# Kernel optimization log

Hardware: AMD Instinct MI355X
Metric: run time of the kernel (lower is better)

Reference implementation:

```python
import jax, jax.numpy as jnp
import numpy as np

N = 65536   # total sentences
B = 8192    # number of bags (ragged scopes)
C = 1024    # class_dim
R = 100     # rel_num


def setup_inputs() -> dict:
    key = jax.random.key(0)
    k1, k2, k3, k4 = jax.random.split(key, 4)
    X = jax.random.normal(k1, (N, C), jnp.float32)            # post-fc1 sentence reps
    Constraints = jax.random.normal(k2, (R, C), jnp.float32)  # post-fc2 constraint reps
    W = jax.random.normal(k3, (R, C), jnp.float32) * 0.02     # classifier weight
    b = jnp.zeros((R,), jnp.float32)                           # classifier bias
    # ragged scopes: random cut points -> contiguous [start, end) per bag
    rng = np.random.default_rng(0)
    cuts = np.sort(rng.choice(np.arange(1, N), B - 1, replace=False))
    starts = np.concatenate([[0], cuts])
    ends = np.concatenate([cuts, [N]])
    X_Scope = jnp.asarray(np.stack([starts, ends], axis=1), jnp.int32)  # [B, 2]
    X_Rel = jax.random.randint(k4, (B,), 0, R, jnp.int32)               # [B]
    return dict(X=X, Constraints=Constraints, W=W, b=b, X_Scope=X_Scope, X_Rel=X_Rel)


def reference(X, Constraints, W, b, X_Scope, X_Rel):
    n, _ = X.shape
    nb = X_Scope.shape[0]
    # map each sentence to its (contiguous) bag via scope starts
    starts = X_Scope[:, 0]
    seg = jnp.searchsorted(starts, jnp.arange(n, dtype=starts.dtype), side='right') - 1  # [N]
    # per-sentence attention logit against its bag's relation constraint
    Con = Constraints[X_Rel]                                   # [B, C]
    scores = jnp.einsum('nc,nc->n', X, Con[seg])               # [N]
    # numerically-stable per-bag softmax
    m = jax.ops.segment_max(scores, seg, num_segments=nb)      # [B]
    e = jnp.exp(scores - m[seg])                               # [N]
    denom = jax.ops.segment_sum(e, seg, num_segments=nb)       # [B]
    w = e / denom[seg]                                         # [N]
    # attention-weighted bag pooling
    bag = jax.ops.segment_sum(w[:, None] * X, seg, num_segments=nb)  # [B, C]
    # classifier (dropout is identity at eval)
    return bag @ W.T + b                                       # [B, R]
```

## Files before the change

### kernel.cpp

```cpp
#include <hip/hip_runtime.h>
#include <math.h>

#define CDIM 1024
#define RDIM 100
#define NBAGS 8192

typedef float floatx4 __attribute__((ext_vector_type(4)));
typedef short bf16x8 __attribute__((ext_vector_type(8)));

__device__ __forceinline__ float dot4(float4 a, float4 b) {
    return a.x * b.x + a.y * b.y + a.z * b.z + a.w * b.w;
}

__device__ __forceinline__ unsigned short f2bf(float f) {
    unsigned int u = __builtin_bit_cast(unsigned int, f);
    u += 0x7FFFu + ((u >> 16) & 1u);
    return (unsigned short)(u >> 16);
}

__global__ __launch_bounds__(256) void bag_softmax_kernel(
    const float* __restrict__ X,
    const float* __restrict__ Constraints,
    const int* __restrict__ scope,
    const int* __restrict__ rel,
    const float* __restrict__ W,
    unsigned short* __restrict__ bagbuf,
    unsigned short* __restrict__ Wbf)
{
    const int lane = threadIdx.x & 63;
    const int w    = threadIdx.x >> 6;

    if (blockIdx.x >= NBAGS) {
        const int rr = blockIdx.x - NBAGS;
        const int t  = threadIdx.x;
        float4 v = *(const float4*)(W + (size_t)rr * CDIM + t * 4);
        ushort4 o;
        o.x = f2bf(v.x); o.y = f2bf(v.y); o.z = f2bf(v.z); o.w = f2bf(v.w);
        *(ushort4*)(Wbf + (size_t)rr * CDIM + t * 4) = o;
        return;
    }

    __shared__ float4 lds_acc[4][256];
    __shared__ float  lds_m[4];
    __shared__ float  lds_d[4];

    const int bag = blockIdx.x;
    const int s = scope[2 * bag];
    const int e = scope[2 * bag + 1];
    const int r = rel[bag];

    const float4* conp = (const float4*)(Constraints + (size_t)r * CDIM);
    const float4 c0 = conp[lane];
    const float4 c1 = conp[lane + 64];
    const float4 c2 = conp[lane + 128];
    const float4 c3 = conp[lane + 192];

    float4 a0 = {0.f, 0.f, 0.f, 0.f};
    float4 a1 = {0.f, 0.f, 0.f, 0.f};
    float4 a2 = {0.f, 0.f, 0.f, 0.f};
    float4 a3 = {0.f, 0.f, 0.f, 0.f};
    float m = -INFINITY;
    float denom = 0.f;

    int row = s + w;
    if (row < e) {
        const float4* xp = (const float4*)(X + (size_t)row * CDIM);
        float4 A0 = xp[lane];
        float4 A1 = xp[lane + 64];
        float4 A2 = xp[lane + 128];
        float4 A3 = xp[lane + 192];

        for (; row < e; row += 4) {
            const int nxt = (row + 4 < e) ? (row + 4) : row;
            const float4* np = (const float4*)(X + (size_t)nxt * CDIM);
            float4 B0 = np[lane];
            float4 B1 = np[lane + 64];
            float4 B2 = np[lane + 128];
            float4 B3 = np[lane + 192];
            __builtin_amdgcn_sched_barrier(0);

            float p = dot4(A0, c0) + dot4(A1, c1) + dot4(A2, c2) + dot4(A3, c3);
            p += __shfl_xor(p, 1);
            p += __shfl_xor(p, 2);
            p += __shfl_xor(p, 4);
            p += __shfl_xor(p, 8);
            p += __shfl_xor(p, 16);
            p += __shfl_xor(p, 32);

            const float newm = fmaxf(m, p);
            const float corr = __expf(m - newm);
            const float wgt  = __expf(p - newm);
            denom = fmaf(denom, corr, wgt);
            a0.x = fmaf(a0.x, corr, wgt * A0.x); a0.y = fmaf(a0.y, corr, wgt * A0.y);
            a0.z = fmaf(a0.z, corr, wgt * A0.z); a0.w = fmaf(a0.w, corr, wgt * A0.w);
            a1.x = fmaf(a1.x, corr, wgt * A1.x); a1.y = fmaf(a1.y, corr, wgt * A1.y);
            a1.z = fmaf(a1.z, corr, wgt * A1.z); a1.w = fmaf(a1.w, corr, wgt * A1.w);
            a2.x = fmaf(a2.x, corr, wgt * A2.x); a2.y = fmaf(a2.y, corr, wgt * A2.y);
            a2.z = fmaf(a2.z, corr, wgt * A2.z); a2.w = fmaf(a2.w, corr, wgt * A2.w);
            a3.x = fmaf(a3.x, corr, wgt * A3.x); a3.y = fmaf(a3.y, corr, wgt * A3.y);
            a3.z = fmaf(a3.z, corr, wgt * A3.z); a3.w = fmaf(a3.w, corr, wgt * A3.w);
            m = newm;

            A0 = B0; A1 = B1; A2 = B2; A3 = B3;
        }
    }

    if (lane == 0) { lds_m[w] = m; lds_d[w] = denom; }
    lds_acc[w][lane]       = a0;
    lds_acc[w][lane + 64]  = a1;
    lds_acc[w][lane + 128] = a2;
    lds_acc[w][lane + 192] = a3;
    __syncthreads();

    const int t = threadIdx.x;
    const float m0 = lds_m[0], m1 = lds_m[1], m2 = lds_m[2], m3 = lds_m[3];
    const float ms = fmaxf(fmaxf(m0, m1), fmaxf(m2, m3));
    const float f0 = __expf(m0 - ms);
    const float f1 = __expf(m1 - ms);
    const float f2 = __expf(m2 - ms);
    const float f3 = __expf(m3 - ms);
    const float dn = f0 * lds_d[0] + f1 * lds_d[1] + f2 * lds_d[2] + f3 * lds_d[3];
    const float inv = 1.0f / dn;

    const float4 v0 = lds_acc[0][t];
    const float4 v1 = lds_acc[1][t];
    const float4 v2 = lds_acc[2][t];
    const float4 v3 = lds_acc[3][t];
    const float ox = (f0 * v0.x + f1 * v1.x + f2 * v2.x + f3 * v3.x) * inv;
    const float oy = (f0 * v0.y + f1 * v1.y + f2 * v2.y + f3 * v3.y) * inv;
    const float oz = (f0 * v0.z + f1 * v1.z + f2 * v2.z + f3 * v3.z) * inv;
    const float ow = (f0 * v0.w + f1 * v1.w + f2 * v2.w + f3 * v3.w) * inv;

    ushort4 o;
    o.x = f2bf(ox); o.y = f2bf(oy); o.z = f2bf(oz); o.w = f2bf(ow);
    *(ushort4*)(bagbuf + (size_t)bag * CDIM + t * 4) = o;
}

__global__ __launch_bounds__(256) void bag_gemm_mfma(
    const unsigned short* __restrict__ bagbuf,
    const unsigned short* __restrict__ Wbf,
    const float* __restrict__ bias,
    float* __restrict__ out)
{
    const int q    = threadIdx.x >> 6;
    const int lane = threadIdx.x & 63;
    const int bag0 = blockIdx.x * 16;
    const int ln15 = lane & 15;
    const int koff = (lane >> 4) * 8;

    __shared__ floatx4 lds[4][7][64];

    floatx4 acc[7];
    #pragma unroll
    for (int t = 0; t < 7; ++t) acc[t] = (floatx4){0.f, 0.f, 0.f, 0.f};

    const unsigned short* aRow = bagbuf + (size_t)(bag0 + ln15) * CDIM + koff;

    #pragma unroll
    for (int i = 0; i < 8; ++i) {
        const int k0 = (q * 8 + i) * 32;
        const bf16x8 a = *(const bf16x8*)(aRow + k0);

        #pragma unroll
        for (int t = 0; t < 7; ++t) {
            const int r = t * 16 + ln15;
            bf16x8 b = (bf16x8)0;
            if (r < RDIM) {
                b = *(const bf16x8*)(Wbf + (size_t)r * CDIM + k0 + koff);
            }
            acc[t] = __builtin_amdgcn_mfma_f32_16x16x32_bf16(a, b, acc[t], 0, 0, 0);
        }
    }

    #pragma unroll
    for (int t = 0; t < 7; ++t) lds[q][t][lane] = acc[t];
    __syncthreads();

    #pragma unroll
    for (int p = threadIdx.x; p < 448; p += 256) {
        const int t    = p >> 6;
        const int slot = p & 63;
        const int r    = t * 16 + (slot & 15);
        if (r < RDIM) {
            floatx4 s = lds[0][t][slot];
            s += lds[1][t][slot];
            s += lds[2][t][slot];
            s += lds[3][t][slot];
            const float bv = bias[r];
            const int bagr = bag0 + (slot >> 4) * 4;
            out[(size_t)(bagr + 0) * RDIM + r] = s[0] + bv;
            out[(size_t)(bagr + 1) * RDIM + r] = s[1] + bv;
            out[(size_t)(bagr + 2) * RDIM + r] = s[2] + bv;
            out[(size_t)(bagr + 3) * RDIM + r] = s[3] + bv;
        }
    }
}

extern "C" void kernel_launch(void* const* d_in, const int* in_sizes, int n_in,
                              void* d_out, int out_size, void* d_ws, size_t ws_size,
                              hipStream_t stream) {
    const float* X    = (const float*)d_in[0];
    const float* Con  = (const float*)d_in[1];
    const float* W    = (const float*)d_in[2];
    const float* bias = (const float*)d_in[3];
    const int* scope  = (const int*)d_in[4];
    const int* rel    = (const int*)d_in[5];
    float* out = (float*)d_out;

    unsigned short* bagbuf = (unsigned short*)d_ws;
    unsigned short* Wbf    = bagbuf + (size_t)NBAGS * CDIM;

    bag_softmax_kernel<<<NBAGS + RDIM, 256, 0, stream>>>(X, Con, scope, rel, W, bagbuf, Wbf);
    bag_gemm_mfma<<<NBAGS / 16, 256, 0, stream>>>(bagbuf, Wbf, bias, out);
}
```

Baseline: 72.26 us.

## Store bag and weight bf16 operands in MFMA fragment order for coalesced GEMM loads

The softmax kernel now writes the bf16 bag vectors and converted weights directly in the per-lane MFMA fragment layout, with weight rows zero-padded to 112. Each GEMM wave can then read a whole fragment with one contiguous 16-byte load per lane, and the row bound check is gone. The GEMM block grows to 512 threads covering two 16-bag tiles, so each block handles 32 bags. Aim: drop strided global reads in the small GEMM; cost is a scattered write pattern in the softmax kernel and 12 extra tiny blocks.

```diff
diff --git a/kernel.cpp b/kernel.cpp
--- a/kernel.cpp
+++ b/kernel.cpp
@@ -4,6 +4,7 @@
 #define CDIM 1024
 #define RDIM 100
 #define NBAGS 8192
+#define RPAD 112
 
 typedef float floatx4 __attribute__((ext_vector_type(4)));
 typedef short bf16x8 __attribute__((ext_vector_type(8)));
@@ -17,6 +18,7 @@
     u += 0x7FFFu + ((u >> 16) & 1u);
     return (unsigned short)(u >> 16);
 }
+
 
 __global__ __launch_bounds__(256) void bag_softmax_kernel(
     const float* __restrict__ X,
@@ -24,8 +26,8 @@
     const int* __restrict__ scope,
     const int* __restrict__ rel,
     const float* __restrict__ W,
-    unsigned short* __restrict__ bagbuf,
-    unsigned short* __restrict__ Wbf)
+    unsigned short* __restrict__ PA,
+    unsigned short* __restrict__ PW)
 {
     const int lane = threadIdx.x & 63;
     const int w    = threadIdx.x >> 6;
@@ -33,10 +35,16 @@
     if (blockIdx.x >= NBAGS) {
         const int rr = blockIdx.x - NBAGS;
         const int t  = threadIdx.x;
-        float4 v = *(const float4*)(W + (size_t)rr * CDIM + t * 4);
-        ushort4 o;
-        o.x = f2bf(v.x); o.y = f2bf(v.y); o.z = f2bf(v.z); o.w = f2bf(v.w);
-        *(ushort4*)(Wbf + (size_t)rr * CDIM + t * 4) = o;
+        const int kc  = t >> 3;
+        const int sub = (t >> 1) & 3;
+        const int i0  = (t & 1) * 4;
+        ushort4 o = {0, 0, 0, 0};
+        if (rr < RDIM) {
+            float4 v = *(const float4*)(W + (size_t)rr * CDIM + t * 4);
+            o.x = f2bf(v.x); o.y = f2bf(v.y); o.z = f2bf(v.z); o.w = f2bf(v.w);
+        }
+        const int tt = rr >> 4, rl = rr & 15;
+        *(ushort4*)(PW + ((size_t)(kc * 7 + tt) * 64 + sub * 16 + rl) * 8 + i0) = o;
         return;
     }
 
@@ -133,61 +141,63 @@
 
     ushort4 o;
     o.x = f2bf(ox); o.y = f2bf(oy); o.z = f2bf(oz); o.w = f2bf(ow);
-    *(ushort4*)(bagbuf + (size_t)bag * CDIM + t * 4) = o;
-}
-
-__global__ __launch_bounds__(256) void bag_gemm_mfma(
-    const unsigned short* __restrict__ bagbuf,
-    const unsigned short* __restrict__ Wbf,
+
+    const int T   = bag >> 4, bl = bag & 15;
+    const int kc  = t >> 3;
+    const int sub = (t >> 1) & 3;
+    const int i0  = (t & 1) * 4;
+    *(ushort4*)(PA + ((size_t)(T * 32 + kc) * 64 + sub * 16 + bl) * 8 + i0) = o;
+}
+
+__global__ __launch_bounds__(512) void bag_gemm_mfma(
+    const unsigned short* __restrict__ PA,
+    const unsigned short* __restrict__ PW,
     const float* __restrict__ bias,
     float* __restrict__ out)
 {
-    const int q    = threadIdx.x >> 6;
+    const int w    = threadIdx.x >> 6;
+    const int q    = w >> 1;
+    const int h    = w & 1;
     const int lane = threadIdx.x & 63;
-    const int bag0 = blockIdx.x * 16;
-    const int ln15 = lane & 15;
-    const int koff = (lane >> 4) * 8;
-
-    __shared__ floatx4 lds[4][7][64];
+    const int T    = blockIdx.x * 2 + h;
+
+    __shared__ floatx4 lds[8][7][64];
 
     floatx4 acc[7];
     #pragma unroll
     for (int t = 0; t < 7; ++t) acc[t] = (floatx4){0.f, 0.f, 0.f, 0.f};
 
-    const unsigned short* aRow = bagbuf + (size_t)(bag0 + ln15) * CDIM + koff;
+    const unsigned short* aBase = PA + ((size_t)T * 32 + q * 8) * 512 + lane * 8;
+    const unsigned short* bBase = PW + (size_t)q * 56 * 512 + lane * 8;
 
     #pragma unroll
     for (int i = 0; i < 8; ++i) {
-        const int k0 = (q * 8 + i) * 32;
-        const bf16x8 a = *(const bf16x8*)(aRow + k0);
-
+        const bf16x8 a = *(const bf16x8*)(aBase + i * 512);
         #pragma unroll
         for (int t = 0; t < 7; ++t) {
-            const int r = t * 16 + ln15;
-            bf16x8 b = (bf16x8)0;
-            if (r < RDIM) {
-                b = *(const bf16x8*)(Wbf + (size_t)r * CDIM + k0 + koff);
-            }
+            const bf16x8 b = *(const bf16x8*)(bBase + (i * 7 + t) * 512);
             acc[t] = __builtin_amdgcn_mfma_f32_16x16x32_bf16(a, b, acc[t], 0, 0, 0);
         }
     }
 
     #pragma unroll
-    for (int t = 0; t < 7; ++t) lds[q][t][lane] = acc[t];
+    for (int t = 0; t < 7; ++t) lds[w][t][lane] = acc[t];
     __syncthreads();
 
     #pragma unroll
-    for (int p = threadIdx.x; p < 448; p += 256) {
-        const int t    = p >> 6;
-        const int slot = p & 63;
+    for (int p = threadIdx.x; p < 896; p += 512) {
+        const int h2   = (p >= 448) ? 1 : 0;
+        const int pp   = p - h2 * 448;
+        const int t    = pp >> 6;
+        const int slot = pp & 63;
         const int r    = t * 16 + (slot & 15);
         if (r < RDIM) {
-            floatx4 s = lds[0][t][slot];
-            s += lds[1][t][slot];
-            s += lds[2][t][slot];
-            s += lds[3][t][slot];
+            floatx4 s = lds[0 + h2][t][slot];
+            s += lds[2 + h2][t][slot];
+            s += lds[4 + h2][t][slot];
+            s += lds[6 + h2][t][slot];
             const float bv = bias[r];
-            const int bagr = bag0 + (slot >> 4) * 4;
+            const int bagr = blockIdx.x * 32 + h2 * 16 + (slot >> 4) * 4;
             out[(size_t)(bagr + 0) * RDIM + r] = s[0] + bv;
             out[(size_t)(bagr + 1) * RDIM + r] = s[1] + bv;
             out[(size_t)(bagr + 2) * RDIM + r] = s[2] + bv;
@@ -207,9 +217,9 @@
     const int* rel    = (const int*)d_in[5];
     float* out = (float*)d_out;
 
-    unsigned short* bagbuf = (unsigned short*)d_ws;
-    unsigned short* Wbf    = bagbuf + (size_t)NBAGS * CDIM;
-
-    bag_softmax_kernel<<<NBAGS + RDIM, 256, 0, stream>>>(X, Con, scope, rel, W, bagbuf, Wbf);
-    bag_gemm_mfma<<<NBAGS / 16, 256, 0, stream>>>(bagbuf, Wbf, bias, out);
-}
+    unsigned short* PA = (unsigned short*)d_ws;
+    unsigned short* PW = PA + (size_t)NBAGS * CDIM;
+
+    bag_softmax_kernel<<<NBAGS + RPAD, 256, 0, stream>>>(X, Con, scope, rel, W, PA, PW);
+    bag_gemm_mfma<<<NBAGS / 32, 512, 0, stream>>>(PA, PW, bias, out);
+}
```

After: 77.61 us. 1.07x slower.
